# Kernel tuning notes

Measured on AMD Instinct MI355X. Metric: run time of the kernel, lower is better.

The kernel has to match this reference:

```python
import jax, jax.numpy as jnp
import numpy as np

HIDDEN = 1024
HEADS = 16
HEAD_DIM = HIDDEN // HEADS

def setup_inputs() -> dict:
    key = jax.random.key(0)
    ks = jax.random.split(key, 11)
    B, T, D = 2, 2048, HIDDEN
    s = 1.0 / np.sqrt(D)
    return {
        "query": jax.random.normal(ks[0], (B, T, D), jnp.float32),
        "key": jax.random.normal(ks[1], (B, T, D), jnp.float32),
        "value": jax.random.normal(ks[2], (B, T, D), jnp.float32),
        "Wq": jax.random.normal(ks[3], (D, D), jnp.float32) * s,
        "bq": jnp.zeros((D,), jnp.float32),
        "Wk": jax.random.normal(ks[4], (D, D), jnp.float32) * s,
        "bk": jnp.zeros((D,), jnp.float32),
        "Wv": jax.random.normal(ks[5], (D, D), jnp.float32) * s,
        "bv": jnp.zeros((D,), jnp.float32),
        "Wo": jax.random.normal(ks[6], (D, D), jnp.float32) * s,
        "bo": jnp.zeros((D,), jnp.float32),
    }

def reference(query, key, value, Wq, bq, Wk, bk, Wv, bv, Wo, bo):
    B, Tq, D = query.shape
    Tk = key.shape[1]
    H, Hd = HEADS, HEAD_DIM
    # projections -> [B, H, T, Hd]
    Q = (query @ Wq + bq).reshape(B, Tq, H, Hd).transpose(0, 2, 1, 3)
    K = (key @ Wk + bk).reshape(B, Tk, H, Hd).transpose(0, 2, 1, 3)
    V = (value @ Wv + bv).reshape(B, Tk, H, Hd).transpose(0, 2, 1, 3)
    scale = jnp.sqrt(jnp.asarray(Hd, Q.dtype))
    scores = jnp.einsum('bhqd,bhkd->bhqk', Q, K) / scale  # [B,H,Tq,Tk]
    causal = jnp.triu(jnp.ones((Tq, Tk), bool), k=1)
    scores = jnp.where(causal[None, None], jnp.asarray(-jnp.inf, scores.dtype), scores)
    attn = jax.nn.softmax(scores, axis=-1)
    out = jnp.einsum('bhqk,bhkd->bhqd', attn, V)  # [B,H,Tq,Hd]
    out = out.transpose(0, 2, 1, 3).reshape(B, Tq, D)
    return out @ Wo + bo
```

## Files before the change

### kernel.cpp

```cpp
#include <hip/hip_runtime.h>
#include <hip/hip_bf16.h>


typedef __bf16 bf16_t;
typedef __bf16 bf16x8 __attribute__((ext_vector_type(8)));
typedef float f32x4 __attribute__((ext_vector_type(4)));
typedef unsigned int u32;

#define D_MODEL 1024
#define SEQ_T   2048
#define NHEAD   16
#define HDIM    64
#define M_ROWS  4096
#define MEGA    (1024 * 1024)

__device__ __forceinline__ void gl2lds16(const void* g, void* l) {
    __builtin_amdgcn_global_load_lds((const __attribute__((address_space(1))) u32*)g,
                                     (__attribute__((address_space(3))) u32*)l, 16, 0, 0);
}

__global__ __launch_bounds__(256) void prep(
    const float* __restrict__ Wq, const float* __restrict__ Wk,
    const float* __restrict__ Wv, const float* __restrict__ Wo,
    const float* __restrict__ Xq, const float* __restrict__ Xk, const float* __restrict__ Xv,
    bf16_t* __restrict__ Wqt, bf16_t* __restrict__ Wkt,
    bf16_t* __restrict__ Wvt, bf16_t* __restrict__ Wot,
    bf16_t* __restrict__ Xb)
{
    int blk = blockIdx.x, tid = threadIdx.x;
    if (blk < 4096) {
        int wi = blk >> 10, t = blk & 1023;
        int n0 = (t & 31) * 32, k0 = (t >> 5) * 32;
        const float* W = wi == 0 ? Wq : (wi == 1 ? Wk : (wi == 2 ? Wv : Wo));
        bf16_t* Wt = wi == 0 ? Wqt : (wi == 1 ? Wkt : (wi == 2 ? Wvt : Wot));
        __shared__ float tile[32][33];
        int tx = tid & 31, ty = tid >> 5;
#pragma unroll
        for (int i = 0; i < 32; i += 8)
            tile[ty + i][tx] = W[(k0 + ty + i) * D_MODEL + n0 + tx];
        __syncthreads();
#pragma unroll
        for (int i = 0; i < 32; i += 8)
            Wt[(size_t)(n0 + ty + i) * D_MODEL + k0 + tx] = (bf16_t)tile[tx][ty + i];
    } else {
        int b2 = blk - 4096;
        int xi = b2 >> 10;
        const float* X = xi == 0 ? Xq : (xi == 1 ? Xk : Xv);
        bf16_t* XB = Xb + (size_t)xi * M_ROWS * D_MODEL;
        size_t base = (size_t)(b2 & 1023) * 4096 + tid * 16;
        const float4* xp = (const float4*)(X + base);
        float4 a0 = xp[0], a1 = xp[1], a2 = xp[2], a3 = xp[3];
        bf16x8 o0, o1;
        o0[0] = (bf16_t)a0.x; o0[1] = (bf16_t)a0.y; o0[2] = (bf16_t)a0.z; o0[3] = (bf16_t)a0.w;
        o0[4] = (bf16_t)a1.x; o0[5] = (bf16_t)a1.y; o0[6] = (bf16_t)a1.z; o0[7] = (bf16_t)a1.w;
        o1[0] = (bf16_t)a2.x; o1[1] = (bf16_t)a2.y; o1[2] = (bf16_t)a2.z; o1[3] = (bf16_t)a2.w;
        o1[4] = (bf16_t)a3.x; o1[5] = (bf16_t)a3.y; o1[6] = (bf16_t)a3.z; o1[7] = (bf16_t)a3.w;
        *(bf16x8*)(XB + base) = o0;
        *(bf16x8*)(XB + base + 8) = o1;
    }
}

template <bool PRECAST>
__global__ __launch_bounds__(256) void proj_fused(
    const float* __restrict__ Xq, const float* __restrict__ Xk, const float* __restrict__ Xv,
    const bf16_t* __restrict__ Xb,
    const bf16_t* __restrict__ Wqt, const bf16_t* __restrict__ Wkt, const bf16_t* __restrict__ Wvt,
    const float* __restrict__ bq, const float* __restrict__ bk, const float* __restrict__ bv,
    bf16_t* __restrict__ Qh, bf16_t* __restrict__ Kh, bf16_t* __restrict__ Vt)
{
    __shared__ bf16_t Ab[128 * 32];
    __shared__ bf16_t Bb[128 * 32];
    int tid = threadIdx.x;
    int w = tid >> 6, lane = tid & 63, lo16 = lane & 15, quad = lane >> 4;
    int m0 = blockIdx.x * 128;
    int proj = blockIdx.y >> 3;
    int n0 = (blockIdx.y & 7) * 128;
    const float*  X    = proj == 0 ? Xq  : (proj == 1 ? Xk  : Xv);
    const bf16_t* XB   = Xb + (size_t)proj * M_ROWS * D_MODEL;
    const bf16_t* Wt   = proj == 0 ? Wqt : (proj == 1 ? Wkt : Wvt);
    const float*  bias = proj == 0 ? bq  : (proj == 1 ? bk  : bv);
    int wm = (w >> 1) * 64, wn = (w & 1) * 64;

    f32x4 acc[4][4];
#pragma unroll
    for (int i = 0; i < 4; i++)
#pragma unroll
        for (int j = 0; j < 4; j++) acc[i][j] = (f32x4){0.f, 0.f, 0.f, 0.f};

    for (int k0 = 0; k0 < D_MODEL; k0 += 32) {
        __syncthreads();
#pragma unroll
        for (int p = 0; p < 2; p++) {
            int idx = p * 256 + tid;
            int row = idx >> 2, ch = (idx & 3) * 8;
            if (PRECAST) {
                gl2lds16(XB + (size_t)(m0 + row) * D_MODEL + k0 + ch, Ab + idx * 8);
            } else {
                const float* as = X + (size_t)(m0 + row) * D_MODEL + k0 + ch;
                float4 a0 = *(const float4*)as, a1 = *(const float4*)(as + 4);
                bf16x8 av;
                av[0] = (bf16_t)a0.x; av[1] = (bf16_t)a0.y; av[2] = (bf16_t)a0.z; av[3] = (bf16_t)a0.w;
                av[4] = (bf16_t)a1.x; av[5] = (bf16_t)a1.y; av[6] = (bf16_t)a1.z; av[7] = (bf16_t)a1.w;
                *(bf16x8*)(Ab + idx * 8) = av;
            }
            gl2lds16(Wt + (size_t)(n0 + row) * D_MODEL + k0 + ch, Bb + idx * 8);
        }
        __syncthreads();
        bf16x8 af[4], bfr[4];
#pragma unroll
        for (int i = 0; i < 4; i++)
            af[i] = *(bf16x8*)(Ab + (wm + i * 16 + lo16) * 32 + quad * 8);
#pragma unroll
        for (int j = 0; j < 4; j++)
            bfr[j] = *(bf16x8*)(Bb + (wn + j * 16 + lo16) * 32 + quad * 8);
#pragma unroll
        for (int i = 0; i < 4; i++)
#pragma unroll
            for (int j = 0; j < 4; j++)
                acc[i][j] = __builtin_amdgcn_mfma_f32_16x16x32_bf16(af[i], bfr[j], acc[i][j], 0, 0, 0);
    }

    float qscale = proj == 0 ? 0.125f : 1.0f;
#pragma unroll
    for (int j = 0; j < 4; j++) {
        int col = n0 + wn + j * 16 + lo16;
        float bv2 = bias[col];
        int h = col >> 6, hd = col & 63;
#pragma unroll
        for (int i = 0; i < 4; i++) {
#pragma unroll
            for (int r = 0; r < 4; r++) {
                int m = m0 + wm + i * 16 + quad * 4 + r;
                int b = m >> 11, t = m & 2047;
                bf16_t val = (bf16_t)((acc[i][j][r] + bv2) * qscale);
                if (proj == 2)
                    Vt[(((size_t)(b * NHEAD + h) * HDIM + hd) * SEQ_T) + t] = val;
                else if (proj == 1)
                    Kh[(((size_t)(b * NHEAD + h) * SEQ_T + t) * HDIM) + hd] = val;
                else
                    Qh[(((size_t)(b * NHEAD + h) * SEQ_T + t) * HDIM) + hd] = val;
            }
        }
    }
}

__global__ __launch_bounds__(128, 2) void flash_attn(const bf16_t* __restrict__ Qh,
                                                     const bf16_t* __restrict__ Kh,
                                                     const bf16_t* __restrict__ Vt,
                                                     bf16_t* __restrict__ Ob) {
    int bh = blockIdx.x & 31;
    int qt = 31 - (int)(blockIdx.x >> 5);
    int tid = threadIdx.x;
    int w = tid >> 6, lane = tid & 63, lo16 = lane & 15, quad = lane >> 4;
    int qbase = qt * 64 + w * 32;

    __shared__ bf16_t KL[64 * 64];
    __shared__ bf16_t VL[64 * 64];
    __shared__ bf16_t PL[2][32 * 64];
    bf16_t* myP = PL[w];

    const bf16_t* Qp = Qh + (size_t)bh * SEQ_T * HDIM;
    const bf16_t* Kp = Kh + (size_t)bh * SEQ_T * HDIM;
    const bf16_t* Vp = Vt + (size_t)bh * HDIM * SEQ_T;

    bf16x8 qf[2][2];
#pragma unroll
    for (int m = 0; m < 2; m++) {
        const bf16_t* qr = Qp + (size_t)(qbase + m * 16 + lo16) * HDIM;
        qf[m][0] = *(const bf16x8*)(qr + quad * 8);
        qf[m][1] = *(const bf16x8*)(qr + 32 + quad * 8);
    }

    bf16x8 ones;
#pragma unroll
    for (int i = 0; i < 8; i++) ones[i] = (bf16_t)1.0f;

    f32x4 oacc[2][4], lacc[2];
#pragma unroll
    for (int m = 0; m < 2; m++) {
        lacc[m] = (f32x4){0.f, 0.f, 0.f, 0.f};
#pragma unroll
        for (int s = 0; s < 4; s++) oacc[m][s] = (f32x4){0.f, 0.f, 0.f, 0.f};
    }

    int nkt = qt + 1;
    for (int kt = 0; kt < nkt; kt++) {
        __syncthreads();
#pragma unroll
        for (int p = 0; p < 4; p++) {
            int idx = p * 128 + tid;
            int row = idx >> 3, cp = idx & 7, cl = (cp - row) & 7;
            gl2lds16(Kp + (size_t)(kt * 64 + row) * HDIM + cl * 8, (bf16_t*)KL + idx * 8);
            gl2lds16(Vp + (size_t)row * SEQ_T + kt * 64 + cl * 8, (bf16_t*)VL + idx * 8);
        }
        __syncthreads();

        f32x4 sacc[2][4];
#pragma unroll
        for (int m = 0; m < 2; m++)
#pragma unroll
            for (int s = 0; s < 4; s++) sacc[m][s] = (f32x4){0.f, 0.f, 0.f, 0.f};
#pragma unroll
        for (int s = 0; s < 4; s++) {
            int keyl = s * 16 + lo16;
            bf16x8 kf0 = *(bf16x8*)(KL + keyl * 64 + ((quad + keyl) & 7) * 8);
            bf16x8 kf1 = *(bf16x8*)(KL + keyl * 64 + ((quad + 4 + keyl) & 7) * 8);
#pragma unroll
            for (int m = 0; m < 2; m++) {
                sacc[m][s] = __builtin_amdgcn_mfma_f32_16x16x32_bf16(qf[m][0], kf0, sacc[m][s], 0, 0, 0);
                sacc[m][s] = __builtin_amdgcn_mfma_f32_16x16x32_bf16(qf[m][1], kf1, sacc[m][s], 0, 0, 0);
            }
        }

        bool diag = (kt == qt);
        bf16x8 pf[2][2];
#pragma unroll
        for (int m = 0; m < 2; m++) {
#pragma unroll
            for (int s = 0; s < 4; s++) {
                int col = s * 16 + lo16;
#pragma unroll
                for (int r = 0; r < 4; r++) {
                    int rowl = m * 16 + quad * 4 + r;
                    float p = __expf(sacc[m][s][r]);
                    if (diag) {
                        int key = kt * 64 + col, qq = qbase + rowl;
                        p = (key <= qq) ? p : 0.f;
                    }
                    int phys = ((col >> 3) + rowl + (rowl >> 3)) & 7;
                    myP[rowl * 64 + phys * 8 + (col & 7)] = (bf16_t)p;
                }
            }
            int rowA = m * 16 + lo16;
            int Rr = (rowA + (rowA >> 3)) & 7;
            pf[m][0] = *(bf16x8*)(myP + rowA * 64 + ((quad + Rr) & 7) * 8);
            pf[m][1] = *(bf16x8*)(myP + rowA * 64 + ((quad + 4 + Rr) & 7) * 8);
            lacc[m] = __builtin_amdgcn_mfma_f32_16x16x32_bf16(pf[m][0], ones, lacc[m], 0, 0, 0);
            lacc[m] = __builtin_amdgcn_mfma_f32_16x16x32_bf16(pf[m][1], ones, lacc[m], 0, 0, 0);
        }

#pragma unroll
        for (int s = 0; s < 4; s++) {
            int dl = s * 16 + lo16;
            bf16x8 vf0 = *(bf16x8*)(VL + dl * 64 + ((quad + dl) & 7) * 8);
            bf16x8 vf1 = *(bf16x8*)(VL + dl * 64 + ((quad + 4 + dl) & 7) * 8);
#pragma unroll
            for (int m = 0; m < 2; m++) {
                oacc[m][s] = __builtin_amdgcn_mfma_f32_16x16x32_bf16(pf[m][0], vf0, oacc[m][s], 0, 0, 0);
                oacc[m][s] = __builtin_amdgcn_mfma_f32_16x16x32_bf16(pf[m][1], vf1, oacc[m][s], 0, 0, 0);
            }
        }
    }

    int b = bh >> 4, h = bh & 15;
#pragma unroll
    for (int m = 0; m < 2; m++)
#pragma unroll
        for (int s = 0; s < 4; s++) {
            int d = s * 16 + lo16;
#pragma unroll
            for (int r = 0; r < 4; r++) {
                int q = qbase + m * 16 + quad * 4 + r;
                float o = oacc[m][s][r] / lacc[m][r];
                Ob[((size_t)b * SEQ_T + q) * D_MODEL + h * HDIM + d] = (bf16_t)o;
            }
        }
}

__global__ __launch_bounds__(256) void out_gemm(const bf16_t* __restrict__ A,
                                                const bf16_t* __restrict__ Wt,
                                                const float* __restrict__ bias,
                                                float* __restrict__ out) {
    __shared__ bf16_t Ab[128 * 32];
    __shared__ bf16_t Bb[128 * 32];
    int tid = threadIdx.x;
    int w = tid >> 6, lane = tid & 63, lo16 = lane & 15, quad = lane >> 4;
    int m0 = blockIdx.x * 128;
    int n0 = blockIdx.y * 128;
    int wm = (w >> 1) * 64, wn = (w & 1) * 64;

    f32x4 acc[4][4];
#pragma unroll
    for (int i = 0; i < 4; i++)
#pragma unroll
        for (int j = 0; j < 4; j++) acc[i][j] = (f32x4){0.f, 0.f, 0.f, 0.f};

    for (int k0 = 0; k0 < D_MODEL; k0 += 32) {
        __syncthreads();
#pragma unroll
        for (int p = 0; p < 2; p++) {
            int idx = p * 256 + tid;
            int row = idx >> 2, ch = (idx & 3) * 8;
            gl2lds16(A  + (size_t)(m0 + row) * D_MODEL + k0 + ch, Ab + idx * 8);
            gl2lds16(Wt + (size_t)(n0 + row) * D_MODEL + k0 + ch, Bb + idx * 8);
        }
        __syncthreads();
        bf16x8 af[4], bfr[4];
#pragma unroll
        for (int i = 0; i < 4; i++)
            af[i] = *(bf16x8*)(Ab + (wm + i * 16 + lo16) * 32 + quad * 8);
#pragma unroll
        for (int j = 0; j < 4; j++)
            bfr[j] = *(bf16x8*)(Bb + (wn + j * 16 + lo16) * 32 + quad * 8);
#pragma unroll
        for (int i = 0; i < 4; i++)
#pragma unroll
            for (int j = 0; j < 4; j++)
                acc[i][j] = __builtin_amdgcn_mfma_f32_16x16x32_bf16(af[i], bfr[j], acc[i][j], 0, 0, 0);
    }

#pragma unroll
    for (int j = 0; j < 4; j++) {
        int col = n0 + wn + j * 16 + lo16;
        float bv2 = bias[col];
#pragma unroll
        for (int i = 0; i < 4; i++)
#pragma unroll
            for (int r = 0; r < 4; r++) {
                int m = m0 + wm + i * 16 + quad * 4 + r;
                out[(size_t)m * D_MODEL + col] = acc[i][j][r] + bv2;
            }
    }
}

extern "C" void kernel_launch(void* const* d_in, const int* in_sizes, int n_in,
                              void* d_out, int out_size, void* d_ws, size_t ws_size,
                              hipStream_t stream) {
    const float* q  = (const float*)d_in[0];
    const float* k  = (const float*)d_in[1];
    const float* v  = (const float*)d_in[2];
    const float* Wq = (const float*)d_in[3];
    const float* bq = (const float*)d_in[4];
    const float* Wk = (const float*)d_in[5];
    const float* bk = (const float*)d_in[6];
    const float* Wv = (const float*)d_in[7];
    const float* bv = (const float*)d_in[8];
    const float* Wo = (const float*)d_in[9];
    const float* bo = (const float*)d_in[10];
    float* out = (float*)d_out;

    bf16_t* Wqt = (bf16_t*)d_ws;
    bf16_t* Wkt = Wqt + (size_t)MEGA;
    bf16_t* Wvt = Wkt + (size_t)MEGA;
    bf16_t* Wot = Wvt + (size_t)MEGA;
    bf16_t* Qh  = Wot + (size_t)MEGA;
    bf16_t* Kh  = Qh  + (size_t)M_ROWS * D_MODEL;
    bf16_t* Vt  = Kh  + (size_t)M_ROWS * D_MODEL;
    bf16_t* Xb  = Vt  + (size_t)M_ROWS * D_MODEL;
    bf16_t* Ob  = Xb;

    bool precast = ws_size >= (size_t)(4 * MEGA + 3 * M_ROWS * D_MODEL + 3 * M_ROWS * D_MODEL) * sizeof(bf16_t);

    int prep_blocks = precast ? 4096 + 3 * 1024 : 4096;
    prep<<<prep_blocks, 256, 0, stream>>>(Wq, Wk, Wv, Wo, q, k, v, Wqt, Wkt, Wvt, Wot, Xb);

    dim3 pg(M_ROWS / 128, 24);
    if (precast)
        proj_fused<true><<<pg, 256, 0, stream>>>(q, k, v, Xb, Wqt, Wkt, Wvt, bq, bk, bv, Qh, Kh, Vt);
    else
        proj_fused<false><<<pg, 256, 0, stream>>>(q, k, v, Xb, Wqt, Wkt, Wvt, bq, bk, bv, Qh, Kh, Vt);

    flash_attn<<<32 * 32, 128, 0, stream>>>(Qh, Kh, Vt, Ob);

    dim3 og(M_ROWS / 128, D_MODEL / 128);
    out_gemm<<<og, 256, 0, stream>>>(Ob, Wot, bo, out);
}
```

Baseline: 229.5 us.

## Use single-wave attention blocks loading K/V fragments directly from global

New measurement: 255.7 us. 11.4% more time.

```diff
diff --git a/kernel.cpp b/kernel.cpp
--- a/kernel.cpp
+++ b/kernel.cpp
@@ -120,7 +120,7 @@
                 acc[i][j] = __builtin_amdgcn_mfma_f32_16x16x32_bf16(af[i], bfr[j], acc[i][j], 0, 0, 0);
     }
 
-    float qscale = proj == 0 ? 0.125f : 1.0f;
+    float qscale = proj == 0 ? 0.1803368801111244f : 1.0f;
 #pragma unroll
     for (int j = 0; j < 4; j++) {
         int col = n0 + wn + j * 16 + lo16;
@@ -144,20 +144,18 @@
     }
 }
 
-__global__ __launch_bounds__(128, 2) void flash_attn(const bf16_t* __restrict__ Qh,
-                                                     const bf16_t* __restrict__ Kh,
-                                                     const bf16_t* __restrict__ Vt,
-                                                     bf16_t* __restrict__ Ob) {
+__global__ __launch_bounds__(64, 2) void flash_attn(const bf16_t* __restrict__ Qh,
+                                                    const bf16_t* __restrict__ Kh,
+                                                    const bf16_t* __restrict__ Vt,
+                                                    bf16_t* __restrict__ Ob) {
     int bh = blockIdx.x & 31;
-    int qt = 31 - (int)(blockIdx.x >> 5);
-    int tid = threadIdx.x;
-    int w = tid >> 6, lane = tid & 63, lo16 = lane & 15, quad = lane >> 4;
-    int qbase = qt * 64 + w * 32;
-
-    __shared__ bf16_t KL[64 * 64];
-    __shared__ bf16_t VL[64 * 64];
-    __shared__ bf16_t PL[2][32 * 64];
-    bf16_t* myP = PL[w];
+    int qt = 63 - (int)(blockIdx.x >> 5);
+    int lane = threadIdx.x;
+    int lo16 = lane & 15, quad = lane >> 4;
+    int qbase = qt * 32;
+
+    __shared__ bf16_t PL[32 * 64];
+    bf16_t* myP = PL;
 
     const bf16_t* Qp = Qh + (size_t)bh * SEQ_T * HDIM;
     const bf16_t* Kp = Kh + (size_t)bh * SEQ_T * HDIM;
@@ -183,18 +181,16 @@
         for (int s = 0; s < 4; s++) oacc[m][s] = (f32x4){0.f, 0.f, 0.f, 0.f};
     }
 
-    int nkt = qt + 1;
+    const bf16_t* krow[4];
+    const bf16_t* vrow[4];
+#pragma unroll
+    for (int s = 0; s < 4; s++) {
+        krow[s] = Kp + (size_t)(s * 16 + lo16) * HDIM + quad * 8;
+        vrow[s] = Vp + (size_t)(s * 16 + lo16) * SEQ_T + quad * 8;
+    }
+
+    int nkt = (qt >> 1) + 1;
     for (int kt = 0; kt < nkt; kt++) {
-        __syncthreads();
-#pragma unroll
-        for (int p = 0; p < 4; p++) {
-            int idx = p * 128 + tid;
-            int row = idx >> 3, cp = idx & 7, cl = (cp - row) & 7;
-            gl2lds16(Kp + (size_t)(kt * 64 + row) * HDIM + cl * 8, (bf16_t*)KL + idx * 8);
-            gl2lds16(Vp + (size_t)row * SEQ_T + kt * 64 + cl * 8, (bf16_t*)VL + idx * 8);
-        }
-        __syncthreads();
-
         f32x4 sacc[2][4];
 #pragma unroll
         for (int m = 0; m < 2; m++)
@@ -202,9 +198,9 @@
             for (int s = 0; s < 4; s++) sacc[m][s] = (f32x4){0.f, 0.f, 0.f, 0.f};
 #pragma unroll
         for (int s = 0; s < 4; s++) {
-            int keyl = s * 16 + lo16;
-            bf16x8 kf0 = *(bf16x8*)(KL + keyl * 64 + ((quad + keyl) & 7) * 8);
-            bf16x8 kf1 = *(bf16x8*)(KL + keyl * 64 + ((quad + 4 + keyl) & 7) * 8);
+            bf16x8 kf0 = *(const bf16x8*)(krow[s]);
+            bf16x8 kf1 = *(const bf16x8*)(krow[s] + 32);
+            krow[s] += 64 * HDIM;
 #pragma unroll
             for (int m = 0; m < 2; m++) {
                 sacc[m][s] = __builtin_amdgcn_mfma_f32_16x16x32_bf16(qf[m][0], kf0, sacc[m][s], 0, 0, 0);
@@ -212,7 +208,15 @@
             }
         }
 
-        bool diag = (kt == qt);
+        bf16x8 vf[4][2];
+#pragma unroll
+        for (int s = 0; s < 4; s++) {
+            vf[s][0] = *(const bf16x8*)(vrow[s]);
+            vf[s][1] = *(const bf16x8*)(vrow[s] + 32);
+            vrow[s] += 64;
+        }
+
+        bool diag = (kt == nkt - 1);
         bf16x8 pf[2][2];
 #pragma unroll
         for (int m = 0; m < 2; m++) {
@@ -222,7 +226,7 @@
 #pragma unroll
                 for (int r = 0; r < 4; r++) {
                     int rowl = m * 16 + quad * 4 + r;
-                    float p = __expf(sacc[m][s][r]);
+                    float p = exp2f(sacc[m][s][r]);
                     if (diag) {
                         int key = kt * 64 + col, qq = qbase + rowl;
                         p = (key <= qq) ? p : 0.f;
@@ -241,13 +245,10 @@
 
 #pragma unroll
         for (int s = 0; s < 4; s++) {
-            int dl = s * 16 + lo16;
-            bf16x8 vf0 = *(bf16x8*)(VL + dl * 64 + ((quad + dl) & 7) * 8);
-            bf16x8 vf1 = *(bf16x8*)(VL + dl * 64 + ((quad + 4 + dl) & 7) * 8);
 #pragma unroll
             for (int m = 0; m < 2; m++) {
-                oacc[m][s] = __builtin_amdgcn_mfma_f32_16x16x32_bf16(pf[m][0], vf0, oacc[m][s], 0, 0, 0);
-                oacc[m][s] = __builtin_amdgcn_mfma_f32_16x16x32_bf16(pf[m][1], vf1, oacc[m][s], 0, 0, 0);
+                oacc[m][s] = __builtin_amdgcn_mfma_f32_16x16x32_bf16(pf[m][0], vf[s][0], oacc[m][s], 0, 0, 0);
+                oacc[m][s] = __builtin_amdgcn_mfma_f32_16x16x32_bf16(pf[m][1], vf[s][1], oacc[m][s], 0, 0, 0);
             }
         }
     }
@@ -360,7 +361,7 @@
     else
         proj_fused<false><<<pg, 256, 0, stream>>>(q, k, v, Xb, Wqt, Wkt, Wvt, bq, bk, bv, Qh, Kh, Vt);
 
-    flash_attn<<<32 * 32, 128, 0, stream>>>(Qh, Kh, Vt, Ob);
+    flash_attn<<<32 * 64, 64, 0, stream>>>(Qh, Kh, Vt, Ob);
 
     dim3 og(M_ROWS / 128, D_MODEL / 128);
     out_gemm<<<og, 256, 0, stream>>>(Ob, Wot, bo, out);
```

## Double-buffer K/V tiles in flash attention with 128-row query blocks

Applied to the files above, without the earlier changes.

Measured after the change: 237.2 us. 1.03x slower.

```diff
diff --git a/kernel.cpp b/kernel.cpp
--- a/kernel.cpp
+++ b/kernel.cpp
@@ -120,7 +120,7 @@
                 acc[i][j] = __builtin_amdgcn_mfma_f32_16x16x32_bf16(af[i], bfr[j], acc[i][j], 0, 0, 0);
     }
 
-    float qscale = proj == 0 ? 0.125f : 1.0f;
+    float qscale = proj == 0 ? 0.1803368801111244f : 1.0f;
 #pragma unroll
     for (int j = 0; j < 4; j++) {
         int col = n0 + wn + j * 16 + lo16;
@@ -144,19 +144,19 @@
     }
 }
 
-__global__ __launch_bounds__(128, 2) void flash_attn(const bf16_t* __restrict__ Qh,
+__global__ __launch_bounds__(256, 2) void flash_attn(const bf16_t* __restrict__ Qh,
                                                      const bf16_t* __restrict__ Kh,
                                                      const bf16_t* __restrict__ Vt,
                                                      bf16_t* __restrict__ Ob) {
     int bh = blockIdx.x & 31;
-    int qt = 31 - (int)(blockIdx.x >> 5);
+    int qt = 15 - (int)(blockIdx.x >> 5);
     int tid = threadIdx.x;
     int w = tid >> 6, lane = tid & 63, lo16 = lane & 15, quad = lane >> 4;
-    int qbase = qt * 64 + w * 32;
-
-    __shared__ bf16_t KL[64 * 64];
-    __shared__ bf16_t VL[64 * 64];
-    __shared__ bf16_t PL[2][32 * 64];
+    int qbase = qt * 128 + w * 32;
+
+    __shared__ bf16_t KL[2][64 * 64];
+    __shared__ bf16_t VL[2][64 * 64];
+    __shared__ bf16_t PL[4][32 * 64];
     bf16_t* myP = PL[w];
 
     const bf16_t* Qp = Qh + (size_t)bh * SEQ_T * HDIM;
@@ -183,17 +183,34 @@
         for (int s = 0; s < 4; s++) oacc[m][s] = (f32x4){0.f, 0.f, 0.f, 0.f};
     }
 
-    int nkt = qt + 1;
+    int nkt = 2 * (qt + 1);
+    int myNkt = 2 * qt + 1 + (w >> 1);
+
+#pragma unroll
+    for (int p = 0; p < 2; p++) {
+        int idx = p * 256 + tid;
+        int row = idx >> 3, cp = idx & 7, cl = (cp - row) & 7;
+        gl2lds16(Kp + (size_t)row * HDIM + cl * 8, KL[0] + idx * 8);
+        gl2lds16(Vp + (size_t)row * SEQ_T + cl * 8, VL[0] + idx * 8);
+    }
+
     for (int kt = 0; kt < nkt; kt++) {
-        __syncthreads();
-#pragma unroll
-        for (int p = 0; p < 4; p++) {
-            int idx = p * 128 + tid;
-            int row = idx >> 3, cp = idx & 7, cl = (cp - row) & 7;
-            gl2lds16(Kp + (size_t)(kt * 64 + row) * HDIM + cl * 8, (bf16_t*)KL + idx * 8);
-            gl2lds16(Vp + (size_t)row * SEQ_T + kt * 64 + cl * 8, (bf16_t*)VL + idx * 8);
-        }
-        __syncthreads();
+        int cur = kt & 1;
+        __syncthreads();
+
+        if (kt + 1 < nkt) {
+#pragma unroll
+            for (int p = 0; p < 2; p++) {
+                int idx = p * 256 + tid;
+                int row = idx >> 3, cp = idx & 7, cl = (cp - row) & 7;
+                gl2lds16(Kp + (size_t)((kt + 1) * 64 + row) * HDIM + cl * 8, KL[cur ^ 1] + idx * 8);
+                gl2lds16(Vp + (size_t)row * SEQ_T + (kt + 1) * 64 + cl * 8, VL[cur ^ 1] + idx * 8);
+            }
+        }
+
+        if (kt >= myNkt) continue;
+        const bf16_t* KLc = KL[cur];
+        const bf16_t* VLc = VL[cur];
 
         f32x4 sacc[2][4];
 #pragma unroll
@@ -203,8 +220,8 @@
 #pragma unroll
         for (int s = 0; s < 4; s++) {
             int keyl = s * 16 + lo16;
-            bf16x8 kf0 = *(bf16x8*)(KL + keyl * 64 + ((quad + keyl) & 7) * 8);
-            bf16x8 kf1 = *(bf16x8*)(KL + keyl * 64 + ((quad + 4 + keyl) & 7) * 8);
+            bf16x8 kf0 = *(const bf16x8*)(KLc + keyl * 64 + ((quad + keyl) & 7) * 8);
+            bf16x8 kf1 = *(const bf16x8*)(KLc + keyl * 64 + ((quad + 4 + keyl) & 7) * 8);
 #pragma unroll
             for (int m = 0; m < 2; m++) {
                 sacc[m][s] = __builtin_amdgcn_mfma_f32_16x16x32_bf16(qf[m][0], kf0, sacc[m][s], 0, 0, 0);
@@ -212,7 +229,7 @@
             }
         }
 
-        bool diag = (kt == qt);
+        bool diag = (kt == myNkt - 1);
         bf16x8 pf[2][2];
 #pragma unroll
         for (int m = 0; m < 2; m++) {
@@ -222,7 +239,7 @@
 #pragma unroll
                 for (int r = 0; r < 4; r++) {
                     int rowl = m * 16 + quad * 4 + r;
-                    float p = __expf(sacc[m][s][r]);
+                    float p = exp2f(sacc[m][s][r]);
                     if (diag) {
                         int key = kt * 64 + col, qq = qbase + rowl;
                         p = (key <= qq) ? p : 0.f;
@@ -242,8 +259,8 @@
 #pragma unroll
         for (int s = 0; s < 4; s++) {
             int dl = s * 16 + lo16;
-            bf16x8 vf0 = *(bf16x8*)(VL + dl * 64 + ((quad + dl) & 7) * 8);
-            bf16x8 vf1 = *(bf16x8*)(VL + dl * 64 + ((quad + 4 + dl) & 7) * 8);
+            bf16x8 vf0 = *(const bf16x8*)(VLc + dl * 64 + ((quad + dl) & 7) * 8);
+            bf16x8 vf1 = *(const bf16x8*)(VLc + dl * 64 + ((quad + 4 + dl) & 7) * 8);
 #pragma unroll
             for (int m = 0; m < 2; m++) {
                 oacc[m][s] = __builtin_amdgcn_mfma_f32_16x16x32_bf16(pf[m][0], vf0, oacc[m][s], 0, 0, 0);
@@ -360,7 +377,7 @@
     else
         proj_fused<false><<<pg, 256, 0, stream>>>(q, k, v, Xb, Wqt, Wkt, Wvt, bq, bk, bv, Qh, Kh, Vt);
 
-    flash_attn<<<32 * 32, 128, 0, stream>>>(Qh, Kh, Vt, Ob);
+    flash_attn<<<32 * 16, 256, 0, stream>>>(Qh, Kh, Vt, Ob);
 
     dim3 og(M_ROWS / 128, D_MODEL / 128);
     out_gemm<<<og, 256, 0, stream>>>(Ob, Wot, bo, out);
```
